# Kernel optimization log

Hardware: AMD Instinct MI355X
Metric: run time of the kernel (lower is better)

The kernel has to match this reference:

```python
import jax, jax.numpy as jnp
import numpy as np

B, S, DM = 2, 2048, 1024
H, KH, HD = 16, 4, 64  # query heads, kv heads, head_dim
N_REP = H // KH


def rotate_half(u):
    d = u.shape[-1] // 2
    return jnp.concatenate([-u[..., d:], u[..., :d]], axis=-1)


def setup_inputs() -> dict:
    key = jax.random.key(0)
    ks = jax.random.split(key, 7)
    x = jax.random.normal(ks[0], (B, S, DM), dtype=jnp.float32)
    # RoPE tables (real rotary angles for realism)
    inv_freq = 1.0 / (10000.0 ** (jnp.arange(0, HD, 2, dtype=jnp.float32) / HD))
    t = jnp.arange(S, dtype=jnp.float32)
    freqs = jnp.outer(t, inv_freq)                      # [S, HD/2]
    emb = jnp.concatenate([freqs, freqs], axis=-1)      # [S, HD]
    cos, sin = jnp.cos(emb), jnp.sin(emb)
    sc = 0.02
    wq = jax.random.normal(ks[1], (DM, H * HD), dtype=jnp.float32) * sc
    wk = jax.random.normal(ks[2], (DM, KH * HD), dtype=jnp.float32) * sc
    wv = jax.random.normal(ks[3], (DM, KH * HD), dtype=jnp.float32) * sc
    wo = jax.random.normal(ks[4], (H * HD, DM), dtype=jnp.float32) * sc
    return {"x": x, "cos": cos, "sin": sin, "wq": wq, "wk": wk, "wv": wv, "wo": wo}


def reference(x, cos, sin, wq, wk, wv, wo):
    b, s, _ = x.shape
    # QKV projections (no bias)
    q = (x @ wq).reshape(b, s, H, HD)   # [b,s,H,HD]
    k = (x @ wk).reshape(b, s, KH, HD)  # [b,s,KH,HD]
    v = (x @ wv).reshape(b, s, KH, HD)
    # RoPE, broadcast cos/sin over the head axis
    c = cos[None, :s, None, :]
    sn = sin[None, :s, None, :]
    q = q * c + rotate_half(q) * sn
    k = k * c + rotate_half(k) * sn
    # GQA: repeat kv heads (repeat_interleave along head axis)
    k = jnp.repeat(k, N_REP, axis=2)  # [b,s,H,HD]
    v = jnp.repeat(v, N_REP, axis=2)
    # causal attention, full score matrix (non-flash path)
    scores = jnp.einsum("bqhd,bkhd->bhqk", q, k) / jnp.sqrt(jnp.float32(HD))
    causal = jnp.tril(jnp.ones((s, s), dtype=bool))
    scores = jnp.where(causal[None, None], scores, jnp.float32(-jnp.inf))
    attn = jax.nn.softmax(scores, axis=-1)
    out = jnp.einsum("bhqk,bkhd->bqhd", attn, v).reshape(b, s, H * HD)
    return out @ wo
```

## Files before the change

kernel.cpp:

```cpp
#include <hip/hip_runtime.h>
#include <hip/hip_bf16.h>

#define BATCH 2
#define SLEN  2048
#define DM    1024
#define NH    16
#define NKH   4
#define HD    64
#define NCH   4
#define PSTRIDE (BATCH * SLEN * NH * HD)
#define LSTRIDE (BATCH * SLEN * NH)

typedef __attribute__((ext_vector_type(8))) short short8;
typedef __attribute__((ext_vector_type(4))) float f32x4;

static __device__ __forceinline__ short f2bf(float x) {
    unsigned u = __float_as_uint(x);
    u += 0x7fffu + ((u >> 16) & 1u);
    return (short)(u >> 16);
}

static __device__ __forceinline__ void ldg_lds16(const short* g, short* l) {
    __builtin_amdgcn_global_load_lds(
        (const __attribute__((address_space(1))) unsigned int*)(const void*)g,
        (__attribute__((address_space(3))) unsigned int*)(void*)l,
        16, 0, 0);
}

#define QSCALE 0.1803368801f

__global__ void cvt_bf16(const float* __restrict__ X, short* __restrict__ Xb, int total8)
{
    const int i = blockIdx.x * blockDim.x + threadIdx.x;
    if (i >= total8) return;
    const float4 v0 = ((const float4*)X)[i * 2];
    const float4 v1 = ((const float4*)X)[i * 2 + 1];
    __align__(16) short o[8];
    o[0] = f2bf(v0.x); o[1] = f2bf(v0.y); o[2] = f2bf(v0.z); o[3] = f2bf(v0.w);
    o[4] = f2bf(v1.x); o[5] = f2bf(v1.y); o[6] = f2bf(v1.z); o[7] = f2bf(v1.w);
    ((int4*)Xb)[i] = *(const int4*)o;
}

__global__ __launch_bounds__(256) void wtrans_all(
    const float* __restrict__ wq, const float* __restrict__ wk,
    const float* __restrict__ wv, const float* __restrict__ wo,
    short* __restrict__ T)
{
    const int by = blockIdx.y;
    const float* W; int Nc, rowoff, ntile;
    if (by < 16)      { W = wq; Nc = 1024; rowoff = 0;    ntile = by; }
    else if (by < 20) { W = wk; Nc = 256;  rowoff = 1024; ntile = by - 16; }
    else if (by < 24) { W = wv; Nc = 256;  rowoff = 1280; ntile = by - 20; }
    else              { W = wo; Nc = 1024; rowoff = 1536; ntile = by - 24; }
    const int kt = blockIdx.x * 64;
    const int nt = ntile * 64;
    const int t  = threadIdx.x;
    __shared__ float tile[64][65];

#pragma unroll
    for (int i = 0; i < 4; ++i) {
        const int r = (t >> 4) + i * 16;
        const int c = (t & 15) * 4;
        const float4 v = *(const float4*)(W + (size_t)(kt + r) * Nc + nt + c);
        tile[r][c + 0] = v.x; tile[r][c + 1] = v.y;
        tile[r][c + 2] = v.z; tile[r][c + 3] = v.w;
    }
    __syncthreads();
#pragma unroll
    for (int i = 0; i < 2; ++i) {
        const int rr = (t >> 3) + i * 32;
        const int cc = (t & 7) * 8;
        __align__(16) short o[8];
#pragma unroll
        for (int j = 0; j < 8; ++j) o[j] = f2bf(tile[cc + j][rr]);
        *(int4*)(T + (size_t)(rowoff + nt + rr) * 1024 + kt + cc) = *(const int4*)o;
    }
}

template<int MODE>
__global__ __launch_bounds__(256) void gemm_abt(
    const short* __restrict__ A, const short* __restrict__ Bt,
    int M, int N, int K,
    float* __restrict__ Cf,
    short* __restrict__ Qb, short* __restrict__ Kb, short* __restrict__ Vb,
    const float* __restrict__ cosp, const float* __restrict__ sinp)
{
    const int t    = threadIdx.x;
    const int lane = t & 63;
    const int w    = t >> 6;
    const int l15  = lane & 15;
    const int l4   = lane >> 4;
    const int n0   = blockIdx.x * 128;
    const int m0   = blockIdx.y * 64;
    const int wm   = (w & 1) * 32;
    const int wn   = (w >> 1) * 64;

    __shared__ __align__(16) short As[64 * 64];
    __shared__ __align__(16) short Bs[128 * 64];

    f32x4 acc[2][4];
#pragma unroll
    for (int i = 0; i < 2; ++i)
#pragma unroll
        for (int j = 0; j < 4; ++j) acc[i][j] = (f32x4){0.f, 0.f, 0.f, 0.f};

    for (int kt = 0; kt < K; kt += 64) {
        __syncthreads();
#pragma unroll
        for (int i = 0; i < 2; ++i) {
            const int chunk = i * 256 + t;
            const int r = chunk >> 3;
            const int c = (chunk & 7) * 8;
            ldg_lds16(A + (size_t)(m0 + r) * K + kt + c, &As[chunk * 8]);
        }
#pragma unroll
        for (int i = 0; i < 4; ++i) {
            const int chunk = i * 256 + t;
            const int r = chunk >> 3;
            const int c = (chunk & 7) * 8;
            ldg_lds16(Bt + (size_t)(n0 + r) * K + kt + c, &Bs[chunk * 8]);
        }
        __syncthreads();

#pragma unroll
        for (int k2 = 0; k2 < 2; ++k2) {
            short8 af[2], bf[4];
#pragma unroll
            for (int i = 0; i < 2; ++i)
                af[i] = *(const short8*)&As[(wm + i * 16 + l15) * 64 + k2 * 32 + l4 * 8];
#pragma unroll
            for (int j = 0; j < 4; ++j)
                bf[j] = *(const short8*)&Bs[(wn + j * 16 + l15) * 64 + k2 * 32 + l4 * 8];
#pragma unroll
            for (int i = 0; i < 2; ++i)
#pragma unroll
                for (int j = 0; j < 4; ++j)
                    acc[i][j] = __builtin_amdgcn_mfma_f32_16x16x32_bf16(af[i], bf[j], acc[i][j], 0, 0, 0);
        }
    }

    if (MODE == 1) {
#pragma unroll
        for (int i = 0; i < 2; ++i)
#pragma unroll
            for (int j = 0; j < 4; ++j)
#pragma unroll
                for (int r = 0; r < 4; ++r) {
                    const int m = m0 + wm + i * 16 + l4 * 4 + r;
                    const int n = n0 + wn + j * 16 + l15;
                    Cf[(size_t)m * N + n] = acc[i][j][r];
                }
        return;
    }

    const int colbase = n0 + wn;
    if (colbase < 1024) {
        const int h = colbase >> 6;
#pragma unroll
        for (int i = 0; i < 2; ++i)
#pragma unroll
            for (int r = 0; r < 4; ++r) {
                const int m = m0 + wm + i * 16 + l4 * 4 + r;
                const int b = m >> 11, s = m & (SLEN - 1);
                short* dst = Qb + (((size_t)(b * SLEN + s) * NH + h) << 6);
#pragma unroll
                for (int j = 0; j < 2; ++j) {
                    const int d = j * 16 + l15;
                    const float cv = cosp[s * HD + d];
                    const float sv = sinp[s * HD + d];
                    const float a0 = acc[i][j][r];
                    const float a1 = acc[i][j + 2][r];
                    dst[d]      = f2bf((a0 * cv - a1 * sv) * QSCALE);
                    dst[d + 32] = f2bf((a1 * cv + a0 * sv) * QSCALE);
                }
            }
    } else if (colbase < 1280) {
        const int kh = (colbase - 1024) >> 6;
#pragma unroll
        for (int i = 0; i < 2; ++i)
#pragma unroll
            for (int r = 0; r < 4; ++r) {
                const int m = m0 + wm + i * 16 + l4 * 4 + r;
                const int b = m >> 11, s = m & (SLEN - 1);
                short* dst = Kb + (((size_t)(b * SLEN + s) * NKH + kh) << 6);
#pragma unroll
                for (int j = 0; j < 2; ++j) {
                    const int d = j * 16 + l15;
                    const float cv = cosp[s * HD + d];
                    const float sv = sinp[s * HD + d];
                    const float a0 = acc[i][j][r];
                    const float a1 = acc[i][j + 2][r];
                    dst[d]      = f2bf(a0 * cv - a1 * sv);
                    dst[d + 32] = f2bf(a1 * cv + a0 * sv);
                }
            }
    } else {
        const int kh = (colbase - 1280) >> 6;
#pragma unroll
        for (int i = 0; i < 2; ++i)
#pragma unroll
            for (int r = 0; r < 4; ++r) {
                const int m = m0 + wm + i * 16 + l4 * 4 + r;
                const int b = m >> 11, s = m & (SLEN - 1);
                short* dst = Vb + (((size_t)(b * SLEN + s) * NKH + kh) << 6);
#pragma unroll
                for (int j = 0; j < 4; ++j)
                    dst[j * 16 + l15] = f2bf(acc[i][j][r]);
            }
    }
}

__global__ __launch_bounds__(256) void vtrans_b(
    const short* __restrict__ Vb, short* __restrict__ Vt)
{
    const int s0 = blockIdx.x * 64;
    const int kh = blockIdx.y;
    const int b  = blockIdx.z;
    const int t  = threadIdx.x;
    __shared__ short tile[64][72];

#pragma unroll
    for (int i = 0; i < 2; ++i) {
        const int chunk = i * 256 + t;
        const int r = chunk >> 3;
        const int c = (chunk & 7) * 8;
        *(int4*)&tile[r][c] =
            *(const int4*)(Vb + (((size_t)(b * SLEN + s0 + r) * NKH + kh) << 6) + c);
    }
    __syncthreads();
#pragma unroll
    for (int i = 0; i < 2; ++i) {
        const int chunk = i * 256 + t;
        const int d  = chunk >> 3;
        const int sc = (chunk & 7) * 8;
        __align__(16) short o[8];
#pragma unroll
        for (int j = 0; j < 8; ++j) {
            const int sp = sc + j;
            const int u  = ((sp & 3) << 4) | (sp >> 2);
            o[j] = tile[u][d];
        }
        *(int4*)(Vt + ((size_t)((b * NKH + kh) * HD + d)) * SLEN + s0 + sc) = *(const int4*)o;
    }
}

#define PSTR 72

__global__ __launch_bounds__(256, 4) void flash_mfma(
    const short* __restrict__ Qb,
    const short* __restrict__ Kb,
    const short* __restrict__ Vt,
    short* __restrict__ O,
    float* __restrict__ Op,
    float* __restrict__ Lp)
{
    const int qs = 63 - blockIdx.x;
    const int kc = blockIdx.y & 3;
    if (kc * 16 > qs) return;
    const int kh = blockIdx.y >> 2;
    const int b  = blockIdx.z;
    const int t    = threadIdx.x;
    const int lane = t & 63;
    const int w    = t >> 6;
    const int h    = kh * 4 + w;
    const int l15  = lane & 15;
    const int l4   = lane >> 4;
    const int q0   = qs * 32;
    const int sw   = l15 & 7;

    __shared__ __align__(16) short Ks[64 * 64];
    __shared__ __align__(16) short Vs[64 * 64];
    __shared__ __align__(16) short Ps[4][32 * PSTR];

    short8 aq[2][2];
#pragma unroll
    for (int i = 0; i < 2; ++i)
#pragma unroll
        for (int ks = 0; ks < 2; ++ks)
            aq[i][ks] = *(const short8*)(
                Qb + ((size_t)((b * SLEN + q0 + i * 16 + l15) * NH + h)) * HD + ks * 32 + l4 * 8);

    f32x4 acc[2][4];
    f32x4 accl[2];
#pragma unroll
    for (int i = 0; i < 2; ++i) {
#pragma unroll
        for (int nt = 0; nt < 4; ++nt) acc[i][nt] = (f32x4){0.f, 0.f, 0.f, 0.f};
        accl[i] = (f32x4){0.f, 0.f, 0.f, 0.f};
    }

    const short8 ones8 = {0x3f80, 0x3f80, 0x3f80, 0x3f80, 0x3f80, 0x3f80, 0x3f80, 0x3f80};

    const int ntiles = (q0 >> 6) + 1;
    const int kt0  = kc * 8;
    const int kend = (kt0 + 8 < ntiles) ? kt0 + 8 : ntiles;

    for (int kt = kt0; kt < kend; ++kt) {
        const int k0 = kt * 64;
        __syncthreads();
#pragma unroll
        for (int i = 0; i < 2; ++i) {
            const int chunk = i * 256 + t;
            const int r  = chunk >> 3;
            const int c8 = chunk & 7;
            const int cs = (c8 ^ (r & 7)) * 8;
            ldg_lds16(Kb + ((size_t)((b * SLEN + k0 + r) * NKH + kh)) * HD + cs,
                      &Ks[chunk * 8]);
            ldg_lds16(Vt + ((size_t)((b * NKH + kh) * HD + r)) * SLEN + k0 + cs,
                      &Vs[chunk * 8]);
        }
        __syncthreads();

        f32x4 sf[2][4];
#pragma unroll
        for (int i = 0; i < 2; ++i)
#pragma unroll
            for (int f = 0; f < 4; ++f) sf[i][f] = (f32x4){0.f, 0.f, 0.f, 0.f};
#pragma unroll
        for (int ks = 0; ks < 2; ++ks)
#pragma unroll
            for (int f = 0; f < 4; ++f) {
                const short8 bk = *(const short8*)
                    &Ks[(f * 16 + l15) * 64 + ((ks * 4 + l4) ^ sw) * 8];
#pragma unroll
                for (int i = 0; i < 2; ++i)
                    sf[i][f] = __builtin_amdgcn_mfma_f32_16x16x32_bf16(aq[i][ks], bk, sf[i][f], 0, 0, 0);
            }

        if (kt == ntiles - 1) {
#pragma unroll
            for (int i = 0; i < 2; ++i)
#pragma unroll
                for (int f = 0; f < 4; ++f)
#pragma unroll
                    for (int r = 0; r < 4; ++r)
                        if (k0 + f * 16 + l15 > q0 + i * 16 + l4 * 4 + r)
                            sf[i][f][r] = -1e30f;
        }

#pragma unroll
        for (int i = 0; i < 2; ++i)
#pragma unroll
            for (int r = 0; r < 4; ++r) {
                __align__(8) short pk[4];
#pragma unroll
                for (int f = 0; f < 4; ++f) pk[f] = f2bf(exp2f(sf[i][f][r]));
                *(int2*)&Ps[w][(i * 16 + l4 * 4 + r) * PSTR + 4 * l15] = *(const int2*)pk;
            }

#pragma unroll
        for (int ks = 0; ks < 2; ++ks) {
            short8 ap[2];
#pragma unroll
            for (int i = 0; i < 2; ++i)
                ap[i] = *(const short8*)&Ps[w][(i * 16 + l15) * PSTR + ks * 32 + l4 * 8];
#pragma unroll
            for (int nt = 0; nt < 4; ++nt) {
                const short8 bv = *(const short8*)
                    &Vs[(nt * 16 + l15) * 64 + ((ks * 4 + l4) ^ sw) * 8];
#pragma unroll
                for (int i = 0; i < 2; ++i)
                    acc[i][nt] = __builtin_amdgcn_mfma_f32_16x16x32_bf16(ap[i], bv, acc[i][nt], 0, 0, 0);
            }
#pragma unroll
            for (int i = 0; i < 2; ++i)
                accl[i] = __builtin_amdgcn_mfma_f32_16x16x32_bf16(ap[i], ones8, accl[i], 0, 0, 0);
        }
    }

    if (q0 < 512) {
#pragma unroll
        for (int i = 0; i < 2; ++i) {
            float rl[4];
#pragma unroll
            for (int r = 0; r < 4; ++r) rl[r] = 1.f / accl[i][r];
#pragma unroll
            for (int nt = 0; nt < 4; ++nt)
#pragma unroll
                for (int r = 0; r < 4; ++r) {
                    const int q = q0 + i * 16 + l4 * 4 + r;
                    O[((size_t)((b * SLEN + q) * NH + h)) * HD + nt * 16 + l15] =
                        f2bf(acc[i][nt][r] * rl[r]);
                }
        }
    } else {
        const size_t pbase = (size_t)kc * PSTRIDE;
#pragma unroll
        for (int i = 0; i < 2; ++i)
#pragma unroll
            for (int nt = 0; nt < 4; ++nt)
#pragma unroll
                for (int r = 0; r < 4; ++r) {
                    const int q = q0 + i * 16 + l4 * 4 + r;
                    Op[pbase + ((size_t)((b * SLEN + q) * NH + h)) * HD + nt * 16 + l15] =
                        acc[i][nt][r];
                }
        if (l15 == 0) {
#pragma unroll
            for (int i = 0; i < 2; ++i)
#pragma unroll
                for (int r = 0; r < 4; ++r) {
                    const int q = q0 + i * 16 + l4 * 4 + r;
                    Lp[(size_t)kc * LSTRIDE + (size_t)(b * SLEN + q) * NH + h] = accl[i][r];
                }
        }
    }
}

__global__ void combine_k(const float* __restrict__ Op, const float* __restrict__ Lp,
                          short* __restrict__ O)
{
    const int idx = blockIdx.x * 256 + threadIdx.x;
    const int dq = idx & 15;
    const int h  = (idx >> 4) & 15;
    const int rr = idx >> 8;
    const int b  = rr / 1536;
    const int s  = 512 + (rr - b * 1536);
    const int nact = (s >> 9) + 1;
    const size_t row = (size_t)(b * SLEN + s) * NH + h;

    float4 o = {0.f, 0.f, 0.f, 0.f};
    float l = 0.f;
    for (int kc = 0; kc < nact; ++kc) {
        const float4 p = *(const float4*)(Op + (size_t)kc * PSTRIDE + row * HD + dq * 4);
        o.x += p.x; o.y += p.y; o.z += p.z; o.w += p.w;
        l += Lp[(size_t)kc * LSTRIDE + row];
    }
    const float rl = 1.f / l;
    __align__(8) short pk[4];
    pk[0] = f2bf(o.x * rl); pk[1] = f2bf(o.y * rl);
    pk[2] = f2bf(o.z * rl); pk[3] = f2bf(o.w * rl);
    *(int2*)(O + row * HD + dq * 4) = *(const int2*)pk;
}

extern "C" void kernel_launch(void* const* d_in, const int* in_sizes, int n_in,
                              void* d_out, int out_size, void* d_ws, size_t ws_size,
                              hipStream_t stream) {
    const float* x    = (const float*)d_in[0];
    const float* cosp = (const float*)d_in[1];
    const float* sinp = (const float*)d_in[2];
    const float* wq   = (const float*)d_in[3];
    const float* wk   = (const float*)d_in[4];
    const float* wv   = (const float*)d_in[5];
    const float* wo   = (const float*)d_in[6];
    float* out = (float*)d_out;

    const int Mrows = BATCH * SLEN;

    short* xb = (short*)d_ws;
    short* Ob = xb;
    short* wT = xb + (size_t)Mrows * 1024;
    short* Qb = wT + (size_t)2560 * 1024;
    short* Kb = Qb + (size_t)Mrows * 1024;
    short* Vt = Kb + (size_t)Mrows * 256;
    short* Vb = Vt + (size_t)Mrows * 256;
    float* Op = (float*)(Vb + (size_t)Mrows * 256);
    float* Lp = Op + (size_t)NCH * PSTRIDE;

    cvt_bf16<<<(Mrows * DM / 8 + 255) / 256, 256, 0, stream>>>(x, xb, Mrows * DM / 8);

    wtrans_all<<<dim3(16, 40), 256, 0, stream>>>(wq, wk, wv, wo, wT);

    gemm_abt<0><<<dim3(1536 / 128, Mrows / 64), 256, 0, stream>>>(
        xb, wT, Mrows, 1536, DM, nullptr, Qb, Kb, Vb, cosp, sinp);

    vtrans_b<<<dim3(SLEN / 64, NKH, BATCH), 256, 0, stream>>>(Vb, Vt);

    flash_mfma<<<dim3(SLEN / 32, NKH * NCH, BATCH), 256, 0, stream>>>(
        Qb, Kb, Vt, Ob, Op, Lp);

    combine_k<<<(BATCH * 1536 * NH * 16) / 256, 256, 0, stream>>>(Op, Lp, Ob);

    gemm_abt<1><<<dim3(DM / 128, Mrows / 64), 256, 0, stream>>>(
        Ob, wT + (size_t)1536 * 1024, Mrows, DM, DM, out,
        nullptr, nullptr, nullptr, nullptr, nullptr);
}
```

Before: 191.2 us.

## Double-buffer K/V tiles in flash attention and fuse x conversion into weight prep

The flash attention kernel now keeps two LDS buffers for K and V. While the MFMAs run on the current tile, the next tile is prefetched with global_load_lds, and one barrier per iteration replaces two. This should hide global load latency behind the score and PV compute. The cost is more shared memory per block, so the launch-bounds occupancy hint drops from 4 to 3 blocks. Separately, the fp32-to-bf16 conversion of x is folded into the weight transpose kernel as extra grid rows, saving one kernel launch.

```diff
diff --git a/kernel.cpp b/kernel.cpp
--- a/kernel.cpp
+++ b/kernel.cpp
@@ -29,24 +29,30 @@
 
 #define QSCALE 0.1803368801f
 
-__global__ void cvt_bf16(const float* __restrict__ X, short* __restrict__ Xb, int total8)
-{
-    const int i = blockIdx.x * blockDim.x + threadIdx.x;
-    if (i >= total8) return;
-    const float4 v0 = ((const float4*)X)[i * 2];
-    const float4 v1 = ((const float4*)X)[i * 2 + 1];
-    __align__(16) short o[8];
-    o[0] = f2bf(v0.x); o[1] = f2bf(v0.y); o[2] = f2bf(v0.z); o[3] = f2bf(v0.w);
-    o[4] = f2bf(v1.x); o[5] = f2bf(v1.y); o[6] = f2bf(v1.z); o[7] = f2bf(v1.w);
-    ((int4*)Xb)[i] = *(const int4*)o;
-}
-
-__global__ __launch_bounds__(256) void wtrans_all(
+__global__ __launch_bounds__(256) void prep_all(
     const float* __restrict__ wq, const float* __restrict__ wk,
     const float* __restrict__ wv, const float* __restrict__ wo,
-    short* __restrict__ T)
+    short* __restrict__ T,
+    const float* __restrict__ X, short* __restrict__ Xb)
 {
     const int by = blockIdx.y;
+    const int t  = threadIdx.x;
+
+    if (by >= 40) {
+        const int blk = (by - 40) * 16 + blockIdx.x;
+#pragma unroll
+        for (int j = 0; j < 16; ++j) {
+            const int i = blk * 4096 + j * 256 + t;
+            const float4 v0 = ((const float4*)X)[i * 2];
+            const float4 v1 = ((const float4*)X)[i * 2 + 1];
+            __align__(16) short o[8];
+            o[0] = f2bf(v0.x); o[1] = f2bf(v0.y); o[2] = f2bf(v0.z); o[3] = f2bf(v0.w);
+            o[4] = f2bf(v1.x); o[5] = f2bf(v1.y); o[6] = f2bf(v1.z); o[7] = f2bf(v1.w);
+            ((int4*)Xb)[i] = *(const int4*)o;
+        }
+        return;
+    }
+
     const float* W; int Nc, rowoff, ntile;
     if (by < 16)      { W = wq; Nc = 1024; rowoff = 0;    ntile = by; }
     else if (by < 20) { W = wk; Nc = 256;  rowoff = 1024; ntile = by - 16; }
@@ -54,7 +60,6 @@
     else              { W = wo; Nc = 1024; rowoff = 1536; ntile = by - 24; }
     const int kt = blockIdx.x * 64;
     const int nt = ntile * 64;
-    const int t  = threadIdx.x;
     __shared__ float tile[64][65];
 
 #pragma unroll
@@ -246,7 +251,7 @@
 
 #define PSTR 72
 
-__global__ __launch_bounds__(256, 4) void flash_mfma(
+__global__ __launch_bounds__(256, 3) void flash_mfma(
     const short* __restrict__ Qb,
     const short* __restrict__ Kb,
     const short* __restrict__ Vt,
@@ -268,9 +273,12 @@
     const int q0   = qs * 32;
     const int sw   = l15 & 7;
 
-    __shared__ __align__(16) short Ks[64 * 64];
-    __shared__ __align__(16) short Vs[64 * 64];
+    __shared__ __align__(16) short Ks[2][64 * 64];
+    __shared__ __align__(16) short Vs[2][64 * 64];
     __shared__ __align__(16) short Ps[4][32 * PSTR];
+
+    const int r_st  = t >> 3;
+    const int c8_st = t & 7;
 
     short8 aq[2][2];
 #pragma unroll
@@ -295,21 +303,26 @@
     const int kt0  = kc * 8;
     const int kend = (kt0 + 8 < ntiles) ? kt0 + 8 : ntiles;
 
+#define STAGE(BI, K0)                                                          \
+    {                                                                          \
+        _Pragma("unroll")                                                      \
+        for (int i_ = 0; i_ < 2; ++i_) {                                       \
+            const int r  = i_ * 32 + r_st;                                     \
+            const int cs = (c8_st ^ (r & 7)) * 8;                              \
+            const int ch = i_ * 256 + t;                                       \
+            ldg_lds16(Kb + ((size_t)((b * SLEN + (K0) + r) * NKH + kh)) * HD + cs, \
+                      &Ks[BI][ch * 8]);                                        \
+            ldg_lds16(Vt + ((size_t)((b * NKH + kh) * HD + r)) * SLEN + (K0) + cs, \
+                      &Vs[BI][ch * 8]);                                        \
+        }                                                                      \
+    }
+
+    STAGE(0, kt0 * 64)
+
     for (int kt = kt0; kt < kend; ++kt) {
-        const int k0 = kt * 64;
+        const int bi = (kt - kt0) & 1;
         __syncthreads();
-#pragma unroll
-        for (int i = 0; i < 2; ++i) {
-            const int chunk = i * 256 + t;
-            const int r  = chunk >> 3;
-            const int c8 = chunk & 7;
-            const int cs = (c8 ^ (r & 7)) * 8;
-            ldg_lds16(Kb + ((size_t)((b * SLEN + k0 + r) * NKH + kh)) * HD + cs,
-                      &Ks[chunk * 8]);
-            ldg_lds16(Vt + ((size_t)((b * NKH + kh) * HD + r)) * SLEN + k0 + cs,
-                      &Vs[chunk * 8]);
-        }
-        __syncthreads();
+        if (kt + 1 < kend) STAGE(bi ^ 1, (kt + 1) * 64)
 
         f32x4 sf[2][4];
 #pragma unroll
@@ -321,13 +334,14 @@
 #pragma unroll
             for (int f = 0; f < 4; ++f) {
                 const short8 bk = *(const short8*)
-                    &Ks[(f * 16 + l15) * 64 + ((ks * 4 + l4) ^ sw) * 8];
+                    &Ks[bi][(f * 16 + l15) * 64 + ((ks * 4 + l4) ^ sw) * 8];
 #pragma unroll
                 for (int i = 0; i < 2; ++i)
                     sf[i][f] = __builtin_amdgcn_mfma_f32_16x16x32_bf16(aq[i][ks], bk, sf[i][f], 0, 0, 0);
             }
 
         if (kt == ntiles - 1) {
+            const int k0 = kt * 64;
 #pragma unroll
             for (int i = 0; i < 2; ++i)
 #pragma unroll
@@ -357,7 +371,7 @@
 #pragma unroll
             for (int nt = 0; nt < 4; ++nt) {
                 const short8 bv = *(const short8*)
-                    &Vs[(nt * 16 + l15) * 64 + ((ks * 4 + l4) ^ sw) * 8];
+                    &Vs[bi][(nt * 16 + l15) * 64 + ((ks * 4 + l4) ^ sw) * 8];
 #pragma unroll
                 for (int i = 0; i < 2; ++i)
                     acc[i][nt] = __builtin_amdgcn_mfma_f32_16x16x32_bf16(ap[i], bv, acc[i][nt], 0, 0, 0);
@@ -457,9 +471,7 @@
     float* Op = (float*)(Vb + (size_t)Mrows * 256);
     float* Lp = Op + (size_t)NCH * PSTRIDE;
 
-    cvt_bf16<<<(Mrows * DM / 8 + 255) / 256, 256, 0, stream>>>(x, xb, Mrows * DM / 8);
-
-    wtrans_all<<<dim3(16, 40), 256, 0, stream>>>(wq, wk, wv, wo, wT);
+    prep_all<<<dim3(16, 48), 256, 0, stream>>>(wq, wk, wv, wo, wT, x, xb);
 
     gemm_abt<0><<<dim3(1536 / 128, Mrows / 64), 256, 0, stream>>>(
         xb, wT, Mrows, 1536, DM, nullptr, Qb, Kb, Vb, cosp, sinp);
```

Result: no change. 187.5 us (-1.9%).
